# Optimization experiments

Hardware: AMD Instinct MI355X
Metric: run time of the kernel (lower is better)

Reference implementation:

```python
import jax, jax.numpy as jnp
import numpy as np


def setup_inputs() -> dict:
    key = jax.random.key(0)
    k1, k2, k3, k4 = jax.random.split(key, 4)
    B, N, d_in, d_out = 8, 2048, 256, 256
    x = jax.random.normal(k1, (B, N, d_in), dtype=jnp.float32)
    adj_hat = jax.random.uniform(k2, (B, N, N), dtype=jnp.float32)
    W = jax.random.normal(k3, (d_out, d_in), dtype=jnp.float32) * (1.0 / np.sqrt(d_in))
    b = jax.random.normal(k4, (d_out,), dtype=jnp.float32) * 0.01
    return {"x": x, "adj_hat": adj_hat, "W": W, "b": b}


def reference(x, adj_hat, W, b):
    # Degrees from adj = adj_hat - I (i.e. without self loops): row sum minus diagonal.
    N = adj_hat.shape[1]
    diag = jnp.diagonal(adj_hat, axis1=-2, axis2=-1)          # [B, N]
    d = adj_hat.sum(axis=-1) - diag                           # [B, N]
    d_inv_sqrt = jnp.power(d, -0.5)                           # [B, N]
    # dad = D^-1/2 @ adj_hat @ D^-1/2  ==  d_i * a_ij * d_j (elementwise broadcast)
    dad = d_inv_sqrt[:, :, None] * adj_hat * d_inv_sqrt[:, None, :]  # [B, N, N]
    h = jnp.einsum('bnd,od->bno', x, W) + b                   # projection [B, N, d_out]
    return jnp.einsum('bnm,bmo->bno', dad, h)                 # [B, N, d_out]
```

## Files before the change

kernel.cpp:

```cpp
#include <hip/hip_runtime.h>
#include <hip/hip_bf16.h>


#define BATCH 8
#define NN    2048
#define DIN   256
#define DOUT  256
#define RTOT  (BATCH * NN)
#define AP    (NN + 32)
#define HP    (RTOT + 32)

typedef short  bf16x8  __attribute__((ext_vector_type(8)));
typedef short  short4v __attribute__((ext_vector_type(4)));
typedef float  f32x4   __attribute__((ext_vector_type(4)));

__device__ __forceinline__ short f2bf(float f) {
    union { float f; unsigned u; } v; v.f = f;
    unsigned r = v.u + 0x7fffu + ((v.u >> 16) & 1u);
    return (short)(r >> 16);
}

__device__ __forceinline__ void gl_lds16(const unsigned short* g, unsigned short* l) {
    __builtin_amdgcn_global_load_lds(
        (const __attribute__((address_space(1))) unsigned int*)g,
        (__attribute__((address_space(3))) unsigned int*)l, 16, 0, 0);
}

__global__ __launch_bounds__(256) void k_degree_cvt(const float* __restrict__ adj,
                                                    float* __restrict__ dis,
                                                    unsigned short* __restrict__ abf) {
    const int row = blockIdx.x;
    const int n = row & (NN - 1);
    const int tid = threadIdx.x;
    const float4* rp4 = (const float4*)(adj + (size_t)row * NN);
    unsigned short* op = abf + (size_t)row * AP;

    float s = 0.f;
#pragma unroll
    for (int i = 0; i < 2; i++) {
        float4 v = rp4[tid + i * 256];
        s += (v.x + v.y) + (v.z + v.w);
        short4v sv = { f2bf(v.x), f2bf(v.y), f2bf(v.z), f2bf(v.w) };
        *(short4v*)(op + 4 * (tid + i * 256)) = sv;
    }
#pragma unroll
    for (int off = 32; off; off >>= 1) s += __shfl_down(s, off);
    __shared__ float red[4];
    if ((tid & 63) == 0) red[tid >> 6] = s;
    __syncthreads();
    if (tid == 0) {
        float tot  = (red[0] + red[1]) + (red[2] + red[3]);
        float diag = ((const float*)rp4)[n];
        dis[row]   = rsqrtf(tot - diag);
    }
}

__global__ __launch_bounds__(256) void k_proj(const float* __restrict__ x,
                                              const float* __restrict__ W,
                                              const float* __restrict__ bias,
                                              const float* __restrict__ dis,
                                              unsigned short* __restrict__ hT) {
    const int mt  = blockIdx.y;
    const int nt  = blockIdx.x;
    const int tid = threadIdx.x;
    const int w = tid >> 6, lane = tid & 63;
    const int wr = w >> 1, wc = w & 1;
    const int l16 = lane & 15, quad = lane >> 4;

    __shared__ short As[128][32];
    __shared__ short Bs[128][32];

    f32x4 acc[4][4];
#pragma unroll
    for (int i = 0; i < 4; i++)
#pragma unroll
        for (int j = 0; j < 4; j++) acc[i][j] = (f32x4){0.f, 0.f, 0.f, 0.f};

    const float4* Wf4 = (const float4*)(W + (size_t)mt * 128 * DIN);
    const float4* Xf4 = (const float4*)(x + (size_t)nt * 128 * DIN);

    for (int kk = 0; kk < DIN / 32; kk++) {
        const int k0 = kk * 32;
        __syncthreads();
#pragma unroll
        for (int it = 0; it < 4; it++) {
            int idx = tid + it * 256;
            int r = idx >> 3, c = idx & 7;
            float4 va = Wf4[(size_t)r * (DIN / 4) + (k0 >> 2) + c];
            float4 vb = Xf4[(size_t)r * (DIN / 4) + (k0 >> 2) + c];
            short4v sa = { f2bf(va.x), f2bf(va.y), f2bf(va.z), f2bf(va.w) };
            short4v sb = { f2bf(vb.x), f2bf(vb.y), f2bf(vb.z), f2bf(vb.w) };
            *(short4v*)&As[r][c * 4] = sa;
            *(short4v*)&Bs[r][c * 4] = sb;
        }
        __syncthreads();
        bf16x8 af[4], bfv[4];
#pragma unroll
        for (int i = 0; i < 4; i++) af[i]  = *(bf16x8*)&As[wr * 64 + i * 16 + l16][quad * 8];
#pragma unroll
        for (int j = 0; j < 4; j++) bfv[j] = *(bf16x8*)&Bs[wc * 64 + j * 16 + l16][quad * 8];
#pragma unroll
        for (int i = 0; i < 4; i++)
#pragma unroll
            for (int j = 0; j < 4; j++)
                acc[i][j] = __builtin_amdgcn_mfma_f32_16x16x32_bf16(af[i], bfv[j], acc[i][j], 0, 0, 0);
    }

#pragma unroll
    for (int i = 0; i < 4; i++) {
        const int orow_base = mt * 128 + wr * 64 + i * 16 + quad * 4;
#pragma unroll
        for (int r = 0; r < 4; r++) {
            const int orow = orow_base + r;
            const float bb = bias[orow];
#pragma unroll
            for (int j = 0; j < 4; j++) {
                const int col = nt * 128 + wc * 64 + j * 16 + l16;
                float v = (acc[i][j][r] + bb) * dis[col];
                hT[(size_t)orow * HP + col] = (unsigned short)f2bf(v);
            }
        }
    }
}

__global__ __launch_bounds__(256, 2) void k_main(const unsigned short* __restrict__ abf,
                                                 const unsigned short* __restrict__ hT,
                                                 const float* __restrict__ dis,
                                                 float* __restrict__ out) {
    const int bx    = blockIdx.x;
    const int b     = bx & 7;
    const int mtile = (bx >> 3) & 31;
    const int ctile = bx >> 8;
    const int n0    = mtile * 64;
    const int tid  = threadIdx.x;
    const int w    = tid >> 6, lane = tid & 63;
    const int l16  = lane & 15, quad = lane >> 4;
    const int lr   = lane >> 2;
    const int lc   = (lane & 3) * 8;

    __shared__ short As[4][64][32];
    __shared__ short Bs[4][128][32];

    const unsigned short* agp  = abf + (size_t)(b * NN + n0 + w * 16 + lr) * AP + lc;
    const unsigned short* bgp0 = hT + (size_t)(ctile * 128 + w * 32 + lr) * HP + b * NN + lc;
    const unsigned short* bgp1 = bgp0 + (size_t)16 * HP;

    f32x4 acc[4][2];
#pragma unroll
    for (int i = 0; i < 4; i++)
#pragma unroll
        for (int j = 0; j < 2; j++) acc[i][j] = (f32x4){0.f, 0.f, 0.f, 0.f};

    for (int g = 0; g < NN / 128; g++) {
#pragma unroll
        for (int s = 0; s < 4; s++) {
            const int ko = g * 128 + s * 32;
            gl_lds16(agp + ko,  (unsigned short*)&As[s][w * 16][0]);
            gl_lds16(bgp0 + ko, (unsigned short*)&Bs[s][w * 32][0]);
            gl_lds16(bgp1 + ko, (unsigned short*)&Bs[s][w * 32 + 16][0]);
        }
        __syncthreads();
#pragma unroll
        for (int s = 0; s < 4; s++) {
            bf16x8 af[4], bfv[2];
#pragma unroll
            for (int i = 0; i < 4; i++) af[i]  = *(bf16x8*)&As[s][i * 16 + l16][quad * 8];
#pragma unroll
            for (int j = 0; j < 2; j++) bfv[j] = *(bf16x8*)&Bs[s][w * 32 + j * 16 + l16][quad * 8];
#pragma unroll
            for (int i = 0; i < 4; i++)
#pragma unroll
                for (int j = 0; j < 2; j++)
                    acc[i][j] = __builtin_amdgcn_mfma_f32_16x16x32_bf16(af[i], bfv[j], acc[i][j], 0, 0, 0);
        }
        __syncthreads();
    }

    const float* disb = dis + (size_t)b * NN;
#pragma unroll
    for (int i = 0; i < 4; i++) {
#pragma unroll
        for (int r = 0; r < 4; r++) {
            const int nrow = n0 + i * 16 + quad * 4 + r;
            const float dn = disb[nrow];
#pragma unroll
            for (int j = 0; j < 2; j++) {
                const int ocol = ctile * 128 + w * 32 + j * 16 + l16;
                out[((size_t)b * NN + nrow) * DOUT + ocol] = dn * acc[i][j][r];
            }
        }
    }
}

extern "C" void kernel_launch(void* const* d_in, const int* in_sizes, int n_in,
                              void* d_out, int out_size, void* d_ws, size_t ws_size,
                              hipStream_t stream) {
    const float* x    = (const float*)d_in[0];
    const float* adj  = (const float*)d_in[1];
    const float* W    = (const float*)d_in[2];
    const float* bias = (const float*)d_in[3];
    float* out = (float*)d_out;

    float* dis = (float*)d_ws;
    unsigned short* hT  = (unsigned short*)((char*)d_ws + 65536);
    unsigned short* abf = (unsigned short*)((char*)d_ws + 65536 + (size_t)DOUT * HP * 2);

    k_degree_cvt<<<RTOT, 256, 0, stream>>>(adj, dis, abf);
    k_proj<<<dim3(128, 2), 256, 0, stream>>>(x, W, bias, dis, hT);
    k_main<<<512, 256, 0, stream>>>(abf, hT, dis, out);
}
```

Before: 259.1 us.

## Double-buffer k_main LDS loads with 512-thread 128x128 tiles

The main aggregation GEMM moves from 256-thread blocks with 64x128 output tiles to 512-thread blocks with 128x128 tiles, halving the grid to 256 blocks. Each K step of 64 now loads into one of two LDS buffers while MFMAs read the other, which hides global load latency and drops one barrier per iteration. The larger tile reuses each A and B element more. The cost is fewer blocks than before, roughly one per CU on a 256-CU part, so there is less latency hiding across blocks.

```diff
diff --git a/kernel.cpp b/kernel.cpp
--- a/kernel.cpp
+++ b/kernel.cpp
@@ -123,27 +123,31 @@
     }
 }
 
-__global__ __launch_bounds__(256, 2) void k_main(const unsigned short* __restrict__ abf,
+__global__ __launch_bounds__(512, 2) void k_main(const unsigned short* __restrict__ abf,
                                                  const unsigned short* __restrict__ hT,
                                                  const float* __restrict__ dis,
                                                  float* __restrict__ out) {
     const int bx    = blockIdx.x;
     const int b     = bx & 7;
-    const int mtile = (bx >> 3) & 31;
-    const int ctile = bx >> 8;
-    const int n0    = mtile * 64;
+    const int mtile = (bx >> 3) & 15;
+    const int ctile = bx >> 7;
+    const int n0    = mtile * 128;
+    const int o0    = ctile * 128;
     const int tid  = threadIdx.x;
     const int w    = tid >> 6, lane = tid & 63;
     const int l16  = lane & 15, quad = lane >> 4;
-    const int lr   = lane >> 2;
-    const int lc   = (lane & 3) * 8;
-
-    __shared__ short As[4][64][32];
-    __shared__ short Bs[4][128][32];
-
-    const unsigned short* agp  = abf + (size_t)(b * NN + n0 + w * 16 + lr) * AP + lc;
-    const unsigned short* bgp0 = hT + (size_t)(ctile * 128 + w * 32 + lr) * HP + b * NN + lc;
-    const unsigned short* bgp1 = bgp0 + (size_t)16 * HP;
+    const int rh   = w >> 2;
+    const int wc   = w & 3;
+    const int sr   = tid >> 2;
+    const int sc   = (tid & 3) * 8;
+
+    __shared__ short As[2][2][128][32];
+    __shared__ short Bs[2][2][128][32];
+
+    const unsigned short* agp = abf + (size_t)(b * NN + n0 + sr) * AP + sc;
+    const unsigned short* bgp = hT + (size_t)(o0 + sr) * HP + b * NN + sc;
+    unsigned short* alp = (unsigned short*)&As[0][0][sr][sc];
+    unsigned short* blp = (unsigned short*)&Bs[0][0][sr][sc];
 
     f32x4 acc[4][2];
 #pragma unroll
@@ -151,41 +155,49 @@
 #pragma unroll
         for (int j = 0; j < 2; j++) acc[i][j] = (f32x4){0.f, 0.f, 0.f, 0.f};
 
-    for (int g = 0; g < NN / 128; g++) {
-#pragma unroll
-        for (int s = 0; s < 4; s++) {
-            const int ko = g * 128 + s * 32;
-            gl_lds16(agp + ko,  (unsigned short*)&As[s][w * 16][0]);
-            gl_lds16(bgp0 + ko, (unsigned short*)&Bs[s][w * 32][0]);
-            gl_lds16(bgp1 + ko, (unsigned short*)&Bs[s][w * 32 + 16][0]);
-        }
+#define STAGE(buf, g) do {                                              \
+        _Pragma("unroll")                                               \
+        for (int _s = 0; _s < 2; _s++) {                                \
+            const int _ko = (g) * 64 + _s * 32;                         \
+            gl_lds16(agp + _ko, alp + ((buf) * 2 + _s) * 4096);         \
+            gl_lds16(bgp + _ko, blp + ((buf) * 2 + _s) * 4096);         \
+        }                                                               \
+    } while (0)
+
+    STAGE(0, 0);
+
+    for (int g = 0; g < NN / 64; g++) {
+        const int cur = g & 1, nxt = cur ^ 1;
         __syncthreads();
-#pragma unroll
-        for (int s = 0; s < 4; s++) {
+        if (g < NN / 64 - 1) STAGE(nxt, g + 1);
+#pragma unroll
+        for (int s = 0; s < 2; s++) {
             bf16x8 af[4], bfv[2];
 #pragma unroll
-            for (int i = 0; i < 4; i++) af[i]  = *(bf16x8*)&As[s][i * 16 + l16][quad * 8];
-#pragma unroll
-            for (int j = 0; j < 2; j++) bfv[j] = *(bf16x8*)&Bs[s][w * 32 + j * 16 + l16][quad * 8];
+            for (int i = 0; i < 4; i++)
+                af[i]  = *(bf16x8*)&As[cur][s][rh * 64 + i * 16 + l16][quad * 8];
+#pragma unroll
+            for (int j = 0; j < 2; j++)
+                bfv[j] = *(bf16x8*)&Bs[cur][s][wc * 32 + j * 16 + l16][quad * 8];
 #pragma unroll
             for (int i = 0; i < 4; i++)
 #pragma unroll
                 for (int j = 0; j < 2; j++)
                     acc[i][j] = __builtin_amdgcn_mfma_f32_16x16x32_bf16(af[i], bfv[j], acc[i][j], 0, 0, 0);
         }
-        __syncthreads();
-    }
+    }
+#undef STAGE
 
     const float* disb = dis + (size_t)b * NN;
 #pragma unroll
     for (int i = 0; i < 4; i++) {
 #pragma unroll
         for (int r = 0; r < 4; r++) {
-            const int nrow = n0 + i * 16 + quad * 4 + r;
+            const int nrow = n0 + rh * 64 + i * 16 + quad * 4 + r;
             const float dn = disb[nrow];
 #pragma unroll
             for (int j = 0; j < 2; j++) {
-                const int ocol = ctile * 128 + w * 32 + j * 16 + l16;
+                const int ocol = o0 + wc * 32 + j * 16 + l16;
                 out[((size_t)b * NN + nrow) * DOUT + ocol] = dn * acc[i][j][r];
             }
         }
@@ -207,5 +219,5 @@
 
     k_degree_cvt<<<RTOT, 256, 0, stream>>>(adj, dis, abf);
     k_proj<<<dim3(128, 2), 256, 0, stream>>>(x, W, bias, dis, hT);
-    k_main<<<512, 256, 0, stream>>>(abf, hT, dis, out);
-}
+    k_main<<<256, 512, 0, stream>>>(abf, hT, dis, out);
+}
```

Result: slower. 269.6 us (+4.1%).
